# Kernel tuning notes

Measured on AMD Instinct MI355X. Metric: run time of the kernel, lower is better.

The kernel has to match this reference:

```python
import jax, jax.numpy as jnp
import numpy as np

S, N, D_IN, D_GNN, E = 8, 50000, 128, 128, 1600000


def setup_inputs() -> dict:
    key = jax.random.key(0)
    k = jax.random.split(key, 7)
    inp = jax.random.normal(k[0], (S, N, D_IN), dtype=jnp.float32)
    edge_index = jax.random.randint(k[1], (2, E), 0, N, dtype=jnp.int64)
    # SAGEConv params: lin_l (neighbor branch, with bias), lin_r (root, no bias)
    s_in = 1.0 / np.sqrt(D_IN)
    W_l = jax.random.uniform(k[2], (D_GNN, D_IN), jnp.float32, -s_in, s_in)
    b_l = jax.random.uniform(k[3], (D_GNN,), jnp.float32, -s_in, s_in)
    W_r = jax.random.uniform(k[4], (D_GNN, D_IN), jnp.float32, -s_in, s_in)
    s_g = 1.0 / np.sqrt(D_GNN)
    W_fc = jax.random.uniform(k[5], (1, D_GNN), jnp.float32, -s_g, s_g)
    b_fc = jax.random.uniform(k[6], (1,), jnp.float32, -s_g, s_g)
    return {"input": inp, "edge_index": edge_index, "W_l": W_l, "b_l": b_l,
            "W_r": W_r, "W_fc": W_fc, "b_fc": b_fc}


def reference(input, edge_index, W_l, b_l, W_r, W_fc, b_fc):
    src, dst = edge_index[0], edge_index[1]
    n = input.shape[1]
    # in-degree for mean aggregation (isolated nodes -> divide by 1, agg stays 0)
    deg = jax.ops.segment_sum(jnp.ones(src.shape[0], input.dtype), dst,
                              num_segments=n)
    deg = jnp.maximum(deg, 1.0)[:, None]

    def step(xt):  # xt: [N, D_IN]
        agg = jax.ops.segment_sum(xt[src], dst, num_segments=n) / deg
        # SAGEConv: lin_l(mean_agg) + lin_r(x)
        return agg @ W_l.T + b_l + xt @ W_r.T  # [N, D_GNN]

    xs = jax.vmap(step)(input)                   # [S, N, D_GNN]
    ys = (xs @ W_fc.T + b_fc)[..., 0]            # [S, N]
    return xs, ys
```

## Files before the change

kernel.cpp:

```cpp
#include <hip/hip_runtime.h>

#define S_STEPS 8
#define D 128

typedef __attribute__((ext_vector_type(4))) float f32x4;
typedef __attribute__((ext_vector_type(4))) short s16x4;
typedef __attribute__((ext_vector_type(8))) short s16x8;

static __device__ __forceinline__ short f2bf(float f) {
    union { float f; unsigned u; } x; x.f = f;
    unsigned r = x.u + 0x7fffu + ((x.u >> 16) & 1u);
    return (short)(r >> 16);
}

__global__ void count_kernel(const int* __restrict__ dst, int* __restrict__ cnt, int E) {
    int e = blockIdx.x * blockDim.x + threadIdx.x;
    if (e < E) atomicAdd(&cnt[dst[e]], 1);
}

__global__ void cvtw_kernel(const float* __restrict__ Wl, const float* __restrict__ Wr,
                            unsigned short* __restrict__ wbf) {
    int i = blockIdx.x * blockDim.x + threadIdx.x;
    if (i < 256 * 128) {
        int j = i >> 7, k = i & 127;
        float v = (j < 128) ? Wl[j * 128 + k] : Wr[(j - 128) * 128 + k];
        wbf[i] = (unsigned short)f2bf(v);
    }
}

__global__ void cvtwcat_kernel(const float* __restrict__ Wl, const float* __restrict__ Wr,
                               unsigned short* __restrict__ wcat) {
    int i = blockIdx.x * blockDim.x + threadIdx.x;
    if (i < 128 * 256) {
        int j = i >> 8, k = i & 255;
        float v = (k < 128) ? Wl[j * 128 + k] : Wr[j * 128 + (k - 128)];
        wcat[i] = (unsigned short)f2bf(v);
    }
}

__global__ __launch_bounds__(256) void cvtx_kernel(const float* __restrict__ x,
    unsigned short* __restrict__ xbf, int N)
{
    const int lane = threadIdx.x & 63;
    const int wv = threadIdx.x >> 6;
    const int node = blockIdx.x * 4 + wv;
    if (node >= N) return;
#pragma unroll
    for (int t = 0; t < S_STEPS; ++t) {
        float2 v = *(const float2*)(x + ((size_t)t * N + node) * 128 + lane * 2);
        ushort2 u;
        u.x = (unsigned short)f2bf(v.x);
        u.y = (unsigned short)f2bf(v.y);
        *(ushort2*)(xbf + ((size_t)node * S_STEPS + t) * 128 + lane * 2) = u;
    }
}

__global__ __launch_bounds__(1024) void scan_kernel(const int* __restrict__ cnt,
                            int* __restrict__ row_ptr,
                            int* __restrict__ fill, float* __restrict__ rdeg,
                            int N, int E) {
    __shared__ int wsum[16];
    __shared__ int woff[16];
    __shared__ int carry_s;
    const int tid = threadIdx.x;
    const int lane = tid & 63;
    const int wv = tid >> 6;
    if (tid == 0) carry_s = 0;
    __syncthreads();
    for (int base = 0; base < N; base += 1024) {
        int i = base + tid;
        int v = (i < N) ? cnt[i] : 0;
        int inc = v;
#pragma unroll
        for (int off = 1; off < 64; off <<= 1) {
            int t = __shfl_up(inc, off);
            if (lane >= off) inc += t;
        }
        if (lane == 63) wsum[wv] = inc;
        __syncthreads();
        if (wv == 0 && lane < 16) {
            int s = wsum[lane];
            int in2 = s;
#pragma unroll
            for (int off = 1; off < 16; off <<= 1) {
                int t = __shfl_up(in2, off);
                if (lane >= off) in2 += t;
            }
            woff[lane] = in2 - s;
        }
        __syncthreads();
        int carry = carry_s;
        int excl = carry + woff[wv] + inc - v;
        if (i < N) {
            row_ptr[i] = excl;
            fill[i] = excl;
            rdeg[i] = 1.0f / (float)((v > 1) ? v : 1);
        }
        __syncthreads();
        if (tid == 1023) carry_s = carry + woff[15] + inc;
        __syncthreads();
    }
    if (tid == 0) row_ptr[N] = E;
}

__global__ void fill_kernel(const int* __restrict__ src, const int* __restrict__ dst,
                            int* __restrict__ fill, int* __restrict__ eidx, int E) {
    int e = blockIdx.x * blockDim.x + threadIdx.x;
    if (e < E) {
        int p = atomicAdd(&fill[dst[e]], 1);
        eidx[p] = src[e];
    }
}

__global__ __launch_bounds__(256) void lin_kernel(const float* __restrict__ x,
    const unsigned short* __restrict__ wbf, const float* __restrict__ bl,
    unsigned short* __restrict__ hbf, float* __restrict__ outb, int N,
    int SF, int tf)
{
    __shared__ __align__(16) short As[64 * 136];
    __shared__ float bls[128];

    const int tid = threadIdx.x;
    const int row0 = blockIdx.x * 64;
    const int lane = tid & 63;
    const int w = tid >> 6;
    const int m = lane & 15;
    const int q = lane >> 4;

    s16x8 bf[4][4];
#pragma unroll
    for (int ct = 0; ct < 4; ++ct) {
#pragma unroll
        for (int kc = 0; kc < 4; ++kc) {
            int col = (w * 4 + ct) * 16 + m;
            bf[ct][kc] = *(const s16x8*)(wbf + (size_t)col * 128 + kc * 32 + q * 8);
        }
    }
    if (tid < 128) bls[tid] = bl[tid];

#pragma unroll
    for (int it = 0; it < 8; ++it) {
        int i = tid + it * 256;
        int r = i >> 5;
        int kq = i & 31;
        int grow = row0 + r;
        float4 v = make_float4(0.f, 0.f, 0.f, 0.f);
        if (grow < N) v = *(const float4*)(x + (size_t)grow * 128 + kq * 4);
        s16x4 a; a.x = f2bf(v.x); a.y = f2bf(v.y); a.z = f2bf(v.z); a.w = f2bf(v.w);
        *(s16x4*)&As[r * 136 + kq * 4] = a;
    }
    __syncthreads();

    f32x4 acc[4][4];
#pragma unroll
    for (int i = 0; i < 4; ++i)
#pragma unroll
        for (int j = 0; j < 4; ++j) acc[i][j] = (f32x4){0.f, 0.f, 0.f, 0.f};

#pragma unroll
    for (int mt = 0; mt < 4; ++mt) {
        s16x8 af[4];
#pragma unroll
        for (int kc = 0; kc < 4; ++kc)
            af[kc] = *(const s16x8*)&As[(mt * 16 + m) * 136 + kc * 32 + q * 8];
#pragma unroll
        for (int ct = 0; ct < 4; ++ct)
#pragma unroll
            for (int kc = 0; kc < 4; ++kc)
                acc[mt][ct] = __builtin_amdgcn_mfma_f32_16x16x32_bf16(
                    af[kc], bf[ct][kc], acc[mt][ct], 0, 0, 0);
    }

    const int colbase = w * 64;
#pragma unroll
    for (int mt = 0; mt < 4; ++mt) {
        const int rowbase = row0 + mt * 16 + q * 4;
#pragma unroll
        for (int ct = 0; ct < 4; ++ct) {
            int col = colbase + ct * 16 + m;
#pragma unroll
            for (int r = 0; r < 4; ++r) {
                int rr = rowbase + r;
                if (rr < N) {
                    if (col < 128) {
                        hbf[((size_t)rr * SF + tf) * 128 + col] =
                            (unsigned short)f2bf(acc[mt][ct][r]);
                    } else {
                        outb[(size_t)rr * 128 + (col - 128)] = acc[mt][ct][r] + bls[col - 128];
                    }
                }
            }
        }
    }
}

#define BF2ACC(u, j) { union { unsigned v; float f; } lo_, hi_; \
    lo_.v = (u) << 16; hi_.v = (u) & 0xffff0000u; \
    acc[j] += lo_.f; acc[(j) + 1] += hi_.f; }
#define ACC8(p, j) { BF2ACC((p).x, (j)); BF2ACC((p).y, (j) + 2); \
    BF2ACC((p).z, (j) + 4); BF2ACC((p).w, (j) + 6); }

__global__ __launch_bounds__(256) void agg8x_kernel(const unsigned short* __restrict__ xbf,
    const int* __restrict__ row_ptr, const int* __restrict__ eidx,
    const float* __restrict__ rdeg, unsigned short* __restrict__ aggx, int N)
{
    const int lane = threadIdx.x & 63;
    const int wv = threadIdx.x >> 6;
    const int node = blockIdx.x * 4 + wv;
    if (node >= N) return;

    const int beg = row_ptr[node];
    const int end = row_ptr[node + 1];

    float acc[16];
#pragma unroll
    for (int j = 0; j < 16; ++j) acc[j] = 0.f;

    const uint4* hb = (const uint4*)xbf;

    int e = beg;
    for (; e + 2 <= end; e += 2) {
        int s0 = eidx[e];
        int s1 = eidx[e + 1];
        const uint4* q0 = hb + (size_t)s0 * 128 + lane * 2;
        const uint4* q1 = hb + (size_t)s1 * 128 + lane * 2;
        uint4 a0 = q0[0];
        uint4 a1 = q0[1];
        uint4 b0 = q1[0];
        uint4 b1 = q1[1];
        ACC8(a0, 0); ACC8(a1, 8);
        ACC8(b0, 0); ACC8(b1, 8);
    }
    if (e < end) {
        int s0 = eidx[e];
        const uint4* q0 = hb + (size_t)s0 * 128 + lane * 2;
        uint4 a0 = q0[0];
        uint4 a1 = q0[1];
        ACC8(a0, 0); ACC8(a1, 8);
    }

    const float rd = rdeg[node];
    unsigned short* orow = aggx + (size_t)node * (S_STEPS * 128) + lane * 16;
    s16x8 o0, o1;
#pragma unroll
    for (int j = 0; j < 8; ++j) {
        o0[j] = f2bf(acc[j] * rd);
        o1[j] = f2bf(acc[8 + j] * rd);
    }
    __builtin_nontemporal_store(o0, (s16x8*)orow);
    __builtin_nontemporal_store(o1, (s16x8*)orow + 1);
}

__global__ __launch_bounds__(256) void lin2_kernel(
    const unsigned short* __restrict__ aggx, const unsigned short* __restrict__ xbf,
    const unsigned short* __restrict__ wcat, const float* __restrict__ bl,
    const float* __restrict__ wfc, const float* __restrict__ bfc,
    float* __restrict__ xs, float* __restrict__ ys, int N)
{
    __shared__ __align__(16) short As[64 * 264];
    __shared__ float bls[128];
    __shared__ float wfs[128];
    __shared__ float part[4][64];

    const int tid = threadIdx.x;
    const int node0 = blockIdx.x * 8;
    const int lane = tid & 63;
    const int w = tid >> 6;
    const int m = lane & 15;
    const int q = lane >> 4;

    s16x8 bf[2][8];
#pragma unroll
    for (int ct = 0; ct < 2; ++ct) {
#pragma unroll
        for (int kc = 0; kc < 8; ++kc) {
            int col = w * 32 + ct * 16 + m;
            bf[ct][kc] = *(const s16x8*)(wcat + (size_t)col * 256 + kc * 32 + q * 8);
        }
    }
    if (tid < 128) { bls[tid] = bl[tid]; wfs[tid] = wfc[tid]; }

#pragma unroll
    for (int it = 0; it < 4; ++it) {
        int c = tid + it * 256;
        int nl = c >> 7;
        int j = c & 127;
        int t = j >> 4;
        int k16 = j & 15;
        int row = nl * 8 + t;
        int node = node0 + nl;
        s16x8 va = (s16x8){0,0,0,0,0,0,0,0};
        s16x8 vx = (s16x8){0,0,0,0,0,0,0,0};
        if (node < N) {
            size_t src = ((size_t)node * S_STEPS + t) * 128 + k16 * 8;
            va = *(const s16x8*)(aggx + src);
            vx = *(const s16x8*)(xbf + src);
        }
        *(s16x8*)&As[row * 264 + k16 * 8] = va;
        *(s16x8*)&As[row * 264 + 128 + k16 * 8] = vx;
    }
    __syncthreads();

    f32x4 acc[4][2];
#pragma unroll
    for (int i = 0; i < 4; ++i)
#pragma unroll
        for (int j = 0; j < 2; ++j) acc[i][j] = (f32x4){0.f, 0.f, 0.f, 0.f};

#pragma unroll
    for (int mt = 0; mt < 4; ++mt) {
        s16x8 af[8];
#pragma unroll
        for (int kc = 0; kc < 8; ++kc)
            af[kc] = *(const s16x8*)&As[(mt * 16 + m) * 264 + kc * 32 + q * 8];
#pragma unroll
        for (int ct = 0; ct < 2; ++ct)
#pragma unroll
            for (int kc = 0; kc < 8; ++kc)
                acc[mt][ct] = __builtin_amdgcn_mfma_f32_16x16x32_bf16(
                    af[kc], bf[ct][kc], acc[mt][ct], 0, 0, 0);
    }

    float pd[4][4];
#pragma unroll
    for (int i = 0; i < 4; ++i)
#pragma unroll
        for (int r = 0; r < 4; ++r) pd[i][r] = 0.f;

    const int colb = w * 32;
#pragma unroll
    for (int mt = 0; mt < 4; ++mt) {
#pragma unroll
        for (int ct = 0; ct < 2; ++ct) {
            int col = colb + ct * 16 + m;
            float blv = bls[col];
            float wfv = wfs[col];
#pragma unroll
            for (int r = 0; r < 4; ++r) {
                int row = mt * 16 + q * 4 + r;
                int node = node0 + (row >> 3);
                int t = row & 7;
                float o = acc[mt][ct][r] + blv;
                if (node < N) xs[((size_t)t * N + node) * 128 + col] = o;
                pd[mt][r] += o * wfv;
            }
        }
    }
#pragma unroll
    for (int off = 1; off < 16; off <<= 1)
#pragma unroll
        for (int mt = 0; mt < 4; ++mt)
#pragma unroll
            for (int r = 0; r < 4; ++r)
                pd[mt][r] += __shfl_xor(pd[mt][r], off);
    if (m == 0) {
#pragma unroll
        for (int mt = 0; mt < 4; ++mt)
#pragma unroll
            for (int r = 0; r < 4; ++r)
                part[w][mt * 16 + q * 4 + r] = pd[mt][r];
    }
    __syncthreads();
    if (tid < 64) {
        int row = tid;
        float v = part[0][row] + part[1][row] + part[2][row] + part[3][row] + bfc[0];
        int node = node0 + (row >> 3);
        int t = row & 7;
        if (node < N) ys[(size_t)t * N + node] = v;
    }
}

__global__ __launch_bounds__(256) void agg_kernel(const unsigned short* __restrict__ hbf,
    const int* __restrict__ row_ptr, const int* __restrict__ eidx,
    const float* __restrict__ rdeg, const float* __restrict__ wfc,
    const float* __restrict__ bfc, float* __restrict__ outb,
    float* __restrict__ ys, int N)
{
    const int lane = threadIdx.x & 63;
    const int wv = threadIdx.x >> 6;
    const int node = blockIdx.x * 4 + wv;
    if (node >= N) return;
    const int g = lane >> 4;
    const int l = lane & 15;
    const int beg = row_ptr[node];
    const int end = row_ptr[node + 1];

    float acc[8];
#pragma unroll
    for (int j = 0; j < 8; ++j) acc[j] = 0.f;

    const unsigned short* hb = hbf + l * 8;
#pragma unroll 2
    for (int e = beg + g; e < end; e += 4) {
        int s = eidx[e];
        uint4 pk = *(const uint4*)(hb + (size_t)s * 128);
        union { unsigned u; float f; } t;
        t.u = pk.x << 16;        acc[0] += t.f;
        t.u = pk.x & 0xffff0000u; acc[1] += t.f;
        t.u = pk.y << 16;        acc[2] += t.f;
        t.u = pk.y & 0xffff0000u; acc[3] += t.f;
        t.u = pk.z << 16;        acc[4] += t.f;
        t.u = pk.z & 0xffff0000u; acc[5] += t.f;
        t.u = pk.w << 16;        acc[6] += t.f;
        t.u = pk.w & 0xffff0000u; acc[7] += t.f;
    }
#pragma unroll
    for (int j = 0; j < 8; ++j) {
        acc[j] += __shfl_xor(acc[j], 16);
        acc[j] += __shfl_xor(acc[j], 32);
    }
    float ax = (g == 0) ? acc[0] : (g == 1) ? acc[2] : (g == 2) ? acc[4] : acc[6];
    float ay = (g == 0) ? acc[1] : (g == 1) ? acc[3] : (g == 2) ? acc[5] : acc[7];

    const int feat = l * 8 + g * 2;
    const float rd = rdeg[node];
    const float2 base = *(const float2*)(outb + (size_t)node * 128 + feat);
    float ox = base.x + ax * rd;
    float oy = base.y + ay * rd;
    *(float2*)(outb + (size_t)node * 128 + feat) = make_float2(ox, oy);

    const float2 wv2 = *(const float2*)(wfc + feat);
    float p = ox * wv2.x + oy * wv2.y;
#pragma unroll
    for (int off = 32; off > 0; off >>= 1) p += __shfl_down(p, off);
    if (lane == 0) ys[node] = p + bfc[0];
}

extern "C" void kernel_launch(void* const* d_in, const int* in_sizes, int n_in,
                              void* d_out, int out_size, void* d_ws, size_t ws_size,
                              hipStream_t stream)
{
    const float* x   = (const float*)d_in[0];
    const int*   ei  = (const int*)d_in[1];
    const float* Wl  = (const float*)d_in[2];
    const float* bl  = (const float*)d_in[3];
    const float* Wr  = (const float*)d_in[4];
    const float* Wfc = (const float*)d_in[5];
    const float* bfc = (const float*)d_in[6];

    const int N = in_sizes[0] / (S_STEPS * D);
    const int E = in_sizes[1] / 2;
    const int* srcp = ei;
    const int* dstp = ei + E;

    char* p = (char*)d_ws;
    auto alloc = [&](size_t bytes) {
        char* r = p;
        p += (bytes + 255) & ~(size_t)255;
        return r;
    };
    int*   cnt     = (int*)alloc((size_t)N * 4);
    int*   row_ptr = (int*)alloc((size_t)(N + 1) * 4);
    int*   fill    = (int*)alloc((size_t)N * 4);
    float* rdeg    = (float*)alloc((size_t)N * 4);
    int*   eidx    = (int*)alloc((size_t)E * 4);
    unsigned short* wmat = (unsigned short*)alloc((size_t)256 * 128 * 2);

    size_t used = (size_t)(p - (char*)d_ws);
    size_t tbl = (size_t)N * S_STEPS * D * 2;
    bool v4 = (ws_size >= used + 2 * tbl + 4096);

    float* xs    = (float*)d_out;
    float* ysall = xs + (size_t)S_STEPS * N * D;

    (void)hipMemsetAsync(cnt, 0, (size_t)N * 4, stream);
    count_kernel<<<(E + 255) / 256, 256, 0, stream>>>(dstp, cnt, E);
    scan_kernel<<<1, 1024, 0, stream>>>(cnt, row_ptr, fill, rdeg, N, E);
    fill_kernel<<<(E + 255) / 256, 256, 0, stream>>>(srcp, dstp, fill, eidx, E);

    if (v4) {
        unsigned short* xbf  = (unsigned short*)alloc(tbl);
        unsigned short* aggx = (unsigned short*)alloc(tbl);
        cvtwcat_kernel<<<128, 256, 0, stream>>>(Wl, Wr, wmat);
        cvtx_kernel<<<(N + 3) / 4, 256, 0, stream>>>(x, xbf, N);
        agg8x_kernel<<<(N + 3) / 4, 256, 0, stream>>>(xbf, row_ptr, eidx, rdeg,
                                                      aggx, N);
        lin2_kernel<<<(N + 7) / 8, 256, 0, stream>>>(aggx, xbf, wmat, bl, Wfc, bfc,
                                                     xs, ysall, N);
    } else {
        unsigned short* hbf = (unsigned short*)alloc((size_t)N * D * 2);
        cvtw_kernel<<<128, 256, 0, stream>>>(Wl, Wr, wmat);
        const int gl = (N + 63) / 64;
        const int ga = (N + 3) / 4;
        for (int t = 0; t < S_STEPS; ++t) {
            const float* xt = x + (size_t)t * N * D;
            float* outb = xs + (size_t)t * N * D;
            lin_kernel<<<gl, 256, 0, stream>>>(xt, wmat, bl, hbf, outb, N, 1, 0);
            agg_kernel<<<ga, 256, 0, stream>>>(hbf, row_ptr, eidx, rdeg, Wfc, bfc,
                                               outb, ysall + (size_t)t * N, N);
        }
    }
}
```

Measured before the change: 1.141 ms.

## Split bf16 feature table into two 4-step halves for cache-resident gather

The node-major bf16 feature table and aggregation output are split into two halves, each holding 4 of the 8 time steps. The gather kernel runs twice, once per half, so each gather pass works on a 51 MB table instead of 102 MB. That smaller working set has a better chance of staying in the last-level cache. The cost is reading the edge list twice and two kernel launches, and the inner loop is now unrolled by 4 edges.

Measured after the change: 1.122 ms. No clear change (-1.7%).

```diff
diff --git a/kernel.cpp b/kernel.cpp
--- a/kernel.cpp
+++ b/kernel.cpp
@@ -39,7 +39,7 @@
 }
 
 __global__ __launch_bounds__(256) void cvtx_kernel(const float* __restrict__ x,
-    unsigned short* __restrict__ xbf, int N)
+    unsigned short* __restrict__ xbfA, unsigned short* __restrict__ xbfB, int N)
 {
     const int lane = threadIdx.x & 63;
     const int wv = threadIdx.x >> 6;
@@ -51,7 +51,8 @@
         ushort2 u;
         u.x = (unsigned short)f2bf(v.x);
         u.y = (unsigned short)f2bf(v.y);
-        *(ushort2*)(xbf + ((size_t)node * S_STEPS + t) * 128 + lane * 2) = u;
+        unsigned short* tb = (t < 4) ? xbfA : xbfB;
+        *(ushort2*)(tb + ((size_t)node * 4 + (t & 3)) * 128 + lane * 2) = u;
     }
 }
 
@@ -200,9 +201,9 @@
 #define ACC8(p, j) { BF2ACC((p).x, (j)); BF2ACC((p).y, (j) + 2); \
     BF2ACC((p).z, (j) + 4); BF2ACC((p).w, (j) + 6); }
 
-__global__ __launch_bounds__(256) void agg8x_kernel(const unsigned short* __restrict__ xbf,
+__global__ __launch_bounds__(256) void agg4x_kernel(const unsigned short* __restrict__ xbfH,
     const int* __restrict__ row_ptr, const int* __restrict__ eidx,
-    const float* __restrict__ rdeg, unsigned short* __restrict__ aggx, int N)
+    const float* __restrict__ rdeg, unsigned short* __restrict__ aggxH, int N)
 {
     const int lane = threadIdx.x & 63;
     const int wv = threadIdx.x >> 6;
@@ -212,47 +213,41 @@
     const int beg = row_ptr[node];
     const int end = row_ptr[node + 1];
 
-    float acc[16];
-#pragma unroll
-    for (int j = 0; j < 16; ++j) acc[j] = 0.f;
-
-    const uint4* hb = (const uint4*)xbf;
+    float acc[8];
+#pragma unroll
+    for (int j = 0; j < 8; ++j) acc[j] = 0.f;
+
+    const uint4* hb = (const uint4*)xbfH;
 
     int e = beg;
-    for (; e + 2 <= end; e += 2) {
+    for (; e + 4 <= end; e += 4) {
         int s0 = eidx[e];
         int s1 = eidx[e + 1];
-        const uint4* q0 = hb + (size_t)s0 * 128 + lane * 2;
-        const uint4* q1 = hb + (size_t)s1 * 128 + lane * 2;
-        uint4 a0 = q0[0];
-        uint4 a1 = q0[1];
-        uint4 b0 = q1[0];
-        uint4 b1 = q1[1];
-        ACC8(a0, 0); ACC8(a1, 8);
-        ACC8(b0, 0); ACC8(b1, 8);
-    }
-    if (e < end) {
+        int s2 = eidx[e + 2];
+        int s3 = eidx[e + 3];
+        uint4 a = hb[(size_t)s0 * 64 + lane];
+        uint4 b = hb[(size_t)s1 * 64 + lane];
+        uint4 c = hb[(size_t)s2 * 64 + lane];
+        uint4 d = hb[(size_t)s3 * 64 + lane];
+        ACC8(a, 0); ACC8(b, 0); ACC8(c, 0); ACC8(d, 0);
+    }
+    for (; e < end; ++e) {
         int s0 = eidx[e];
-        const uint4* q0 = hb + (size_t)s0 * 128 + lane * 2;
-        uint4 a0 = q0[0];
-        uint4 a1 = q0[1];
-        ACC8(a0, 0); ACC8(a1, 8);
+        uint4 a = hb[(size_t)s0 * 64 + lane];
+        ACC8(a, 0);
     }
 
     const float rd = rdeg[node];
-    unsigned short* orow = aggx + (size_t)node * (S_STEPS * 128) + lane * 16;
-    s16x8 o0, o1;
-#pragma unroll
-    for (int j = 0; j < 8; ++j) {
-        o0[j] = f2bf(acc[j] * rd);
-        o1[j] = f2bf(acc[8 + j] * rd);
-    }
-    __builtin_nontemporal_store(o0, (s16x8*)orow);
-    __builtin_nontemporal_store(o1, (s16x8*)orow + 1);
+    unsigned short* orow = aggxH + ((size_t)node * 4 + (lane >> 4)) * 128 + (lane & 15) * 8;
+    s16x8 o;
+#pragma unroll
+    for (int j = 0; j < 8; ++j) o[j] = f2bf(acc[j] * rd);
+    __builtin_nontemporal_store(o, (s16x8*)orow);
 }
 
 __global__ __launch_bounds__(256) void lin2_kernel(
-    const unsigned short* __restrict__ aggx, const unsigned short* __restrict__ xbf,
+    const unsigned short* __restrict__ aggxA, const unsigned short* __restrict__ aggxB,
+    const unsigned short* __restrict__ xbfA, const unsigned short* __restrict__ xbfB,
     const unsigned short* __restrict__ wcat, const float* __restrict__ bl,
     const float* __restrict__ wfc, const float* __restrict__ bfc,
     float* __restrict__ xs, float* __restrict__ ys, int N)
@@ -292,9 +287,11 @@
         s16x8 va = (s16x8){0,0,0,0,0,0,0,0};
         s16x8 vx = (s16x8){0,0,0,0,0,0,0,0};
         if (node < N) {
-            size_t src = ((size_t)node * S_STEPS + t) * 128 + k16 * 8;
-            va = *(const s16x8*)(aggx + src);
-            vx = *(const s16x8*)(xbf + src);
+            const unsigned short* at = (t < 4) ? aggxA : aggxB;
+            const unsigned short* xt = (t < 4) ? xbfA : xbfB;
+            size_t src = ((size_t)node * 4 + (t & 3)) * 128 + k16 * 8;
+            va = *(const s16x8*)(at + src);
+            vx = *(const s16x8*)(xt + src);
         }
         *(s16x8*)&As[row * 264 + k16 * 8] = va;
         *(s16x8*)&As[row * 264 + 128 + k16 * 8] = vx;
@@ -457,8 +454,8 @@
     unsigned short* wmat = (unsigned short*)alloc((size_t)256 * 128 * 2);
 
     size_t used = (size_t)(p - (char*)d_ws);
-    size_t tbl = (size_t)N * S_STEPS * D * 2;
-    bool v4 = (ws_size >= used + 2 * tbl + 4096);
+    size_t htbl = (size_t)N * 4 * D * 2;
+    bool v5 = (ws_size >= used + 4 * htbl + 4096);
 
     float* xs    = (float*)d_out;
     float* ysall = xs + (size_t)S_STEPS * N * D;
@@ -468,14 +465,19 @@
     scan_kernel<<<1, 1024, 0, stream>>>(cnt, row_ptr, fill, rdeg, N, E);
     fill_kernel<<<(E + 255) / 256, 256, 0, stream>>>(srcp, dstp, fill, eidx, E);
 
-    if (v4) {
-        unsigned short* xbf  = (unsigned short*)alloc(tbl);
-        unsigned short* aggx = (unsigned short*)alloc(tbl);
+    if (v5) {
+        unsigned short* xbfA  = (unsigned short*)alloc(htbl);
+        unsigned short* xbfB  = (unsigned short*)alloc(htbl);
+        unsigned short* aggxA = (unsigned short*)alloc(htbl);
+        unsigned short* aggxB = (unsigned short*)alloc(htbl);
         cvtwcat_kernel<<<128, 256, 0, stream>>>(Wl, Wr, wmat);
-        cvtx_kernel<<<(N + 3) / 4, 256, 0, stream>>>(x, xbf, N);
-        agg8x_kernel<<<(N + 3) / 4, 256, 0, stream>>>(xbf, row_ptr, eidx, rdeg,
-                                                      aggx, N);
-        lin2_kernel<<<(N + 7) / 8, 256, 0, stream>>>(aggx, xbf, wmat, bl, Wfc, bfc,
+        cvtx_kernel<<<(N + 3) / 4, 256, 0, stream>>>(x, xbfA, xbfB, N);
+        agg4x_kernel<<<(N + 3) / 4, 256, 0, stream>>>(xbfA, row_ptr, eidx, rdeg,
+                                                      aggxA, N);
+        agg4x_kernel<<<(N + 3) / 4, 256, 0, stream>>>(xbfB, row_ptr, eidx, rdeg,
+                                                      aggxB, N);
+        lin2_kernel<<<(N + 7) / 8, 256, 0, stream>>>(aggxA, aggxB, xbfA, xbfB,
+                                                     wmat, bl, Wfc, bfc,
                                                      xs, ysall, N);
     } else {
         unsigned short* hbf = (unsigned short*)alloc((size_t)N * D * 2);
```
